# Kernel tuning notes

Measured on AMD Instinct MI355X. Metric: run time of the kernel, lower is better.

Reference implementation:

```python
import jax, jax.numpy as jnp
import numpy as np

DIM = 512  # word_hidden_size * 2


def _linear_params(key, din, dout, scale=0.05):
    kw, kb = jax.random.split(key)
    W = jax.random.normal(kw, (din, dout), dtype=jnp.float32) * scale
    b = jax.random.normal(kb, (dout,), dtype=jnp.float32) * scale
    return W, b


def setup_inputs() -> dict:
    key = jax.random.key(0)
    ks = jax.random.split(key, 16)
    S_c, S_q, B = 256, 32, 32
    inp = {
        'context_output': jax.random.normal(ks[0], (S_c, B, DIM), dtype=jnp.float32),
        'question_output': jax.random.normal(ks[1], (S_q, B, DIM), dtype=jnp.float32),
        'question_hidden_state': jax.random.normal(ks[2], (B, DIM), dtype=jnp.float32),
        'image_output': jax.random.normal(ks[3], (S_c, B, DIM), dtype=jnp.float32),
    }
    names = ['fc1', 'fc2', 'dm', 'rm', 'qm', 'rr', 'rg', 'qg']
    for i, n in enumerate(names):
        W, b = _linear_params(ks[4 + i], DIM, DIM)
        inp['W_' + n] = W
        inp['b_' + n] = b
    W_ms, b_ms = _linear_params(ks[12], DIM, 1)
    inp['W_ms'] = W_ms
    inp['b_ms'] = b_ms
    return inp


def reference(context_output, question_output, question_hidden_state, image_output,
              W_fc1, b_fc1, W_fc2, b_fc2, W_dm, b_dm, W_rm, b_rm, W_qm, b_qm,
              W_rr, b_rr, W_rg, b_rg, W_qg, b_qg, W_ms, b_ms):
    # ctx: [B, S, D] = fc1(context) + fc2(image) after seq-first -> batch-first permute
    ctx = (jnp.einsum('sbd,de->bse', context_output, W_fc1) + b_fc1
           + jnp.einsum('sbd,de->bse', image_output, W_fc2) + b_fc2)
    # hoist loop-invariant linear_dm(ctx): same math, computed once
    ctx_dm = jnp.einsum('bsd,de->bse', ctx, W_dm) + b_dm  # [B, S, D]

    B = ctx.shape[0]
    r0 = jnp.zeros((B, DIM), dtype=ctx.dtype)

    def step(r, q_t):  # r: [B, D], q_t: [B, D]
        rm = r @ W_rm + b_rm          # [B, D]
        qm = q_t @ W_qm + b_qm        # [B, D]
        m = jnp.tanh(ctx_dm + rm[:, None, :] + qm[:, None, :])  # [B, S, D]
        logits = jnp.einsum('bsd,do->bso', m, W_ms)[..., 0] + b_ms[0]  # [B, S]
        s = jax.nn.softmax(logits, axis=1)                     # [B, S]
        r_new = jnp.einsum('bs,bsd->bd', s, ctx) + jnp.tanh(r @ W_rr + b_rr)
        return r_new, None

    r, _ = jax.lax.scan(step, r0, question_output)  # scan over question tokens

    g = (r @ W_rg + b_rg) + (question_hidden_state @ W_qg + b_qg)  # [B, D]
    return g
```

## Files before the change

### kernel.cpp

```cpp
#include <hip/hip_runtime.h>
#include <hip/hip_bf16.h>

#define DIMD 512
#define NB   32
#define NS   256
#define NT   32
#define SA_STR  66
#define SCT_STR 258
#define SR_STR  132

typedef __bf16 bf16x8 __attribute__((ext_vector_type(8)));
typedef float  f32x4  __attribute__((ext_vector_type(4)));
typedef unsigned long long u64;

__device__ __forceinline__ float tanh_fast(float x) {
    float e = __expf(2.f * x);
    return 1.f - 2.f / (e + 1.f);
}

__device__ __forceinline__ void gl_lds16(const __bf16* g, __bf16* l) {
    __builtin_amdgcn_global_load_lds((const __attribute__((address_space(1))) void*)g,
                                     (__attribute__((address_space(3))) void*)l, 16, 0, 0);
}

__device__ __forceinline__ void pub64(u64* p, float v, unsigned tag) {
    u64 pk = ((u64)__float_as_uint(v) << 32) | (u64)tag;
    __hip_atomic_store(p, pk, __ATOMIC_RELAXED, __HIP_MEMORY_SCOPE_AGENT);
}
__device__ __forceinline__ float poll64(const u64* p, unsigned tag) {
    u64 v = __hip_atomic_load(p, __ATOMIC_RELAXED, __HIP_MEMORY_SCOPE_AGENT);
    while ((unsigned)v != tag) {
        __builtin_amdgcn_s_sleep(1);
        v = __hip_atomic_load(p, __ATOMIC_RELAXED, __HIP_MEMORY_SCOPE_AGENT);
    }
    return __uint_as_float((unsigned)(v >> 32));
}

__global__ void k_prep_all(const float* __restrict__ ctxin, const float* __restrict__ img,
                           const float* __restrict__ qin,
                           const float* __restrict__ Wfc1, const float* __restrict__ Wfc2,
                           const float* __restrict__ Wdm, const float* __restrict__ Wqm,
                           const float* __restrict__ Wrm, const float* __restrict__ Wrr,
                           const float* __restrict__ Wrg, const float* __restrict__ Wqg,
                           __bf16* __restrict__ acat, __bf16* __restrict__ qp,
                           __bf16* __restrict__ wcatT, __bf16* __restrict__ wdmT,
                           __bf16* __restrict__ wqmT, __bf16* __restrict__ wrmT,
                           __bf16* __restrict__ wrrT, __bf16* __restrict__ wrgT,
                           __bf16* __restrict__ wqgT) {
    int row = blockIdx.x;
    if (row < 8192) {
        int b = row >> 8, s = row & 255;
        const float* c  = ctxin + ((size_t)s * NB + b) * DIMD;
        const float* im = img   + ((size_t)s * NB + b) * DIMD;
        __bf16* o = acat + (size_t)row * 1024;
        for (int d = threadIdx.x; d < DIMD; d += 256) {
            o[d]       = (__bf16)c[d];
            o[512 + d] = (__bf16)im[d];
        }
    } else if (row < 10240) {
        int idx = (row - 8192) * 256 + threadIdx.x;
        qp[idx] = (__bf16)qin[idx];
    } else {
        __shared__ float tile[32][33];
        int zz = (row - 10240) >> 8;
        int idx = (row - 10240) & 255;
        int bx = idx & 15, by = idx >> 4;
        int x = threadIdx.x & 31, y = threadIdx.x >> 5;
        const float* src = (zz == 0) ? Wfc1 : (zz == 1) ? Wfc2 : (zz == 2) ? Wdm
                         : (zz == 3) ? Wqm : (zz == 4) ? Wrm : (zz == 5) ? Wrr
                         : (zz == 6) ? Wrg : Wqg;
        __bf16* dst; int stride, off;
        if (zz < 2) { dst = wcatT; stride = 1024; off = zz * 512; }
        else {
            dst = (zz == 2) ? wdmT : (zz == 3) ? wqmT : (zz == 4) ? wrmT
                : (zz == 5) ? wrrT : (zz == 6) ? wrgT : wqgT;
            stride = 512; off = 0;
        }
        int c0 = bx * 32, r0 = by * 32;
#pragma unroll
        for (int k = 0; k < 32; k += 8)
            tile[y + k][x] = src[(size_t)(r0 + y + k) * DIMD + c0 + x];
        __syncthreads();
#pragma unroll
        for (int k = 0; k < 32; k += 8)
            dst[(size_t)(c0 + y + k) * stride + off + r0 + x] = (__bf16)tile[x][y + k];
    }
}

__device__ __forceinline__ void gemm_tile128(const __bf16* __restrict__ A,
                                             const __bf16* __restrict__ BT,
                                             const float* __restrict__ bias1,
                                             const float* __restrict__ bias2,
                                             void* __restrict__ out, int N, int K,
                                             int m0, int n0, int out_f32,
                                             __bf16* As, __bf16* Bs) {
    int tid = threadIdx.x, wave = tid >> 6, lane = tid & 63;
    int wm_ = wave >> 1, wn = wave & 1;
    int lr = lane & 15, lq = lane >> 4;

    f32x4 acc[4][4];
#pragma unroll
    for (int i = 0; i < 4; i++)
#pragma unroll
        for (int j = 0; j < 4; j++) acc[i][j] = (f32x4){0.f, 0.f, 0.f, 0.f};

    int g0 = (wave * 2 + 0) * 64 + lane;
    int g1 = (wave * 2 + 1) * 64 + lane;
    int r0_ = g0 >> 2, c0_ = g0 & 3;
    int r1_ = g1 >> 2, c1_ = g1 & 3;
    __bf16* la0 = As + (wave * 2 + 0) * 512;
    __bf16* la1 = As + (wave * 2 + 1) * 512;
    __bf16* lb0 = Bs + (wave * 2 + 0) * 512;
    __bf16* lb1 = Bs + (wave * 2 + 1) * 512;

    for (int kk = 0; kk < K; kk += 32) {
        gl_lds16(A  + (size_t)(m0 + r0_) * K + kk + c0_ * 8, la0);
        gl_lds16(A  + (size_t)(m0 + r1_) * K + kk + c1_ * 8, la1);
        gl_lds16(BT + (size_t)(n0 + r0_) * K + kk + c0_ * 8, lb0);
        gl_lds16(BT + (size_t)(n0 + r1_) * K + kk + c1_ * 8, lb1);
        __syncthreads();
        bf16x8 af[4], bfv[4];
#pragma unroll
        for (int i = 0; i < 4; i++)
            af[i] = *(const bf16x8*)(As + (wm_ * 64 + i * 16 + lr) * 32 + lq * 8);
#pragma unroll
        for (int j = 0; j < 4; j++)
            bfv[j] = *(const bf16x8*)(Bs + (wn * 64 + j * 16 + lr) * 32 + lq * 8);
#pragma unroll
        for (int i = 0; i < 4; i++)
#pragma unroll
            for (int j = 0; j < 4; j++)
                acc[i][j] = __builtin_amdgcn_mfma_f32_16x16x32_bf16(af[i], bfv[j], acc[i][j], 0, 0, 0);
        __syncthreads();
    }

#pragma unroll
    for (int i = 0; i < 4; i++)
#pragma unroll
        for (int j = 0; j < 4; j++) {
            int col = n0 + wn * 64 + j * 16 + lr;
            float bs = (bias1 ? bias1[col] : 0.f) + (bias2 ? bias2[col] : 0.f);
#pragma unroll
            for (int r = 0; r < 4; r++) {
                int row = m0 + wm_ * 64 + i * 16 + lq * 4 + r;
                float v = acc[i][j][r] + bs;
                if (out_f32) ((float*)out)[(size_t)row * N + col] = v;
                else         ((__bf16*)out)[(size_t)row * N + col] = (__bf16)v;
            }
        }
}

__global__ void k_gemm128(const __bf16* __restrict__ A, const __bf16* __restrict__ BT,
                          const float* __restrict__ bias1, const float* __restrict__ bias2,
                          void* __restrict__ out, int M, int N, int K, int out_f32) {
    __shared__ __bf16 As[128 * 32];
    __shared__ __bf16 Bs[128 * 32];
    gemm_tile128(A, BT, bias1, bias2, out, N, K, blockIdx.x * 128, blockIdx.y * 128, out_f32, As, Bs);
}

__global__ void k_fused(const __bf16* __restrict__ ctxb, const __bf16* __restrict__ wdmT,
                        const float* __restrict__ bdm, __bf16* __restrict__ ctxdm,
                        const __bf16* __restrict__ qp, const __bf16* __restrict__ wqmT,
                        const float* __restrict__ bqm, float* __restrict__ qmf,
                        __bf16* __restrict__ ctxT) {
    __shared__ __bf16 As[128 * 32];
    __shared__ __bf16 Bs[128 * 32];
    int bid = blockIdx.x;
    if (bid < 256) {
        gemm_tile128(ctxb, wdmT, bdm, nullptr, ctxdm, 512, 512,
                     (bid & 63) * 128, (bid >> 6) * 128, 0, As, Bs);
    } else if (bid < 288) {
        int b2 = bid - 256;
        gemm_tile128(qp, wqmT, bqm, nullptr, qmf, 512, 512,
                     (b2 & 7) * 128, (b2 >> 3) * 128, 1, As, Bs);
    } else {
        int b3 = bid - 288;
        int z = b3 >> 7, rest = b3 & 127;
        int c0 = (rest & 15) * 32, s0 = (rest >> 4) * 32;
        __bf16* tile = As;
        int x = threadIdx.x & 31, y = threadIdx.x >> 5;
        const __bf16* S = ctxb + (size_t)z * NS * DIMD;
        __bf16* D = ctxT + (size_t)z * DIMD * NS;
#pragma unroll
        for (int k = 0; k < 32; k += 8)
            tile[(y + k) * 33 + x] = S[(size_t)(s0 + y + k) * DIMD + c0 + x];
        __syncthreads();
#pragma unroll
        for (int k = 0; k < 32; k += 8)
            D[(size_t)(c0 + y + k) * NS + s0 + x] = tile[x * 33 + y + k];
    }
}

__global__ __launch_bounds__(512, 2) void k_scan(
    const __bf16* __restrict__ ctxdm,
    const __bf16* __restrict__ ctxT,
    const __bf16* __restrict__ wrmT,
    const __bf16* __restrict__ wrrT,
    const float* __restrict__ qmf,
    const float* __restrict__ wms, const float* __restrict__ brm,
    const float* __restrict__ brr,
    const float* __restrict__ qh,
    const __bf16* __restrict__ wrgT,
    const __bf16* __restrict__ wqgT,
    const float* __restrict__ brg, const float* __restrict__ bqg,
    u64* parts,
    u64* rpub,
    float* __restrict__ out) {
    int bid = blockIdx.x;
    int b = bid & 31, j = bid >> 5;
    int tid = threadIdx.x, wave = tid >> 6, lane = tid & 63;
    int g = lane >> 3, i = lane & 7;

    __shared__ __bf16 sA[256 * SA_STR];
    __shared__ __bf16 sCT[64 * SCT_STR];
    __shared__ float  sQ[NT * 64];
    __shared__ float  sq[512];
    __shared__ float  sp[256];
    __shared__ float  s4[4];
    __shared__ float  sps[8 * 68];
    __shared__ float  srm[64], sh[64];
    __shared__ float  sr4[4 * SR_STR];
    __shared__ float  sqh4[4 * SR_STR];
    __shared__ float  smv[512];

    for (int c = tid; c < 2048; c += 512) {
        int row = c >> 3, c8 = c & 7;
        *(bf16x8*)(sA + row * SA_STR + c8 * 8) =
            *(const bf16x8*)(ctxdm + ((size_t)(b * NS + row)) * DIMD + j * 64 + c8 * 8);
    }
    for (int c = tid; c < 2048; c += 512) {
        int col = c >> 5, s8 = c & 31;
        *(bf16x8*)(sCT + col * SCT_STR + s8 * 8) =
            *(const bf16x8*)(ctxT + ((size_t)(b * DIMD) + j * 64 + col) * NS + s8 * 8);
    }
    for (int c = tid; c < NT * 64; c += 512) {
        int tt = c >> 6, e = c & 63;
        sQ[c] = qmf[((size_t)tt * NB + b) * DIMD + j * 64 + e];
    }
    sqh4[(tid >> 7) * SR_STR + (tid & 127)] = qh[(size_t)b * DIMD + tid];
    int m = tid >> 8, cl = (tid >> 2) & 63, q = tid & 3;
    const __bf16* wp = (m ? wrrT : wrmT) + ((size_t)(j * 64 + cl)) * DIMD + q * 128;
    bf16x8 wreg[16];
#pragma unroll
    for (int u = 0; u < 16; u++) wreg[u] = *(const bf16x8*)(wp + u * 8);

    float wm[8];
#pragma unroll
    for (int u = 0; u < 8; u++) wm[u] = wms[j * 64 + i * 8 + u];
    if (tid < 64) {
        srm[tid] = brm[j * 64 + tid];
        sh[tid]  = tanh_fast(brr[j * 64 + tid]);
    }
    __syncthreads();

    for (int t = 0; t < NT; t++) {
        unsigned tag = (unsigned)(t + 1);
        float rq[8];
#pragma unroll
        for (int u = 0; u < 8; u++) rq[u] = srm[i * 8 + u] + sQ[t * 64 + i * 8 + u];
#pragma unroll
        for (int k = 0; k < 4; k++) {
            int s = wave * 32 + k * 8 + g;
            bf16x8 cv = *(const bf16x8*)(sA + s * SA_STR + i * 8);
            float a = 0.f;
#pragma unroll
            for (int u = 0; u < 8; u++)
                a += tanh_fast((float)cv[u] + rq[u]) * wm[u];
            a += __shfl_xor(a, 1); a += __shfl_xor(a, 2); a += __shfl_xor(a, 4);
            if (i == 0) pub64(&parts[(b * 8 + j) * NS + s], a, tag);
        }

        {
            int s = tid >> 1, jh = (tid & 1) * 4;
            const u64* p0 = &parts[(b * 8 + jh + 0) * NS + s];
            const u64* p1 = &parts[(b * 8 + jh + 1) * NS + s];
            const u64* p2 = &parts[(b * 8 + jh + 2) * NS + s];
            const u64* p3 = &parts[(b * 8 + jh + 3) * NS + s];
            u64 v0, v1, v2, v3;
            for (;;) {
                v0 = __hip_atomic_load(p0, __ATOMIC_RELAXED, __HIP_MEMORY_SCOPE_AGENT);
                v1 = __hip_atomic_load(p1, __ATOMIC_RELAXED, __HIP_MEMORY_SCOPE_AGENT);
                v2 = __hip_atomic_load(p2, __ATOMIC_RELAXED, __HIP_MEMORY_SCOPE_AGENT);
                v3 = __hip_atomic_load(p3, __ATOMIC_RELAXED, __HIP_MEMORY_SCOPE_AGENT);
                if ((unsigned)v0 == tag && (unsigned)v1 == tag &&
                    (unsigned)v2 == tag && (unsigned)v3 == tag) break;
                __builtin_amdgcn_s_sleep(1);
            }
            sq[tid] = __uint_as_float((unsigned)(v0 >> 32)) + __uint_as_float((unsigned)(v1 >> 32))
                    + __uint_as_float((unsigned)(v2 >> 32)) + __uint_as_float((unsigned)(v3 >> 32));
        }
        __syncthreads();
        float ev = 0.f;
        if (tid < NS) { ev = __expf(sq[2 * tid] + sq[2 * tid + 1]); sp[tid] = ev; }
#pragma unroll
        for (int off = 32; off; off >>= 1) ev += __shfl_xor(ev, off);
        if (tid < NS && lane == 0) s4[wave] = ev;
        __syncthreads();
        float inv = 1.f / (s4[0] + s4[1] + s4[2] + s4[3]);
        {
            const __bf16* cp = sCT + lane * SCT_STR + wave * 32;
            const float* pp = sp + wave * 32;
            float a = 0.f;
#pragma unroll
            for (int k = 0; k < 32; k += 8) {
                bf16x8 v = *(const bf16x8*)(cp + k);
#pragma unroll
                for (int u = 0; u < 8; u++) a = fmaf(pp[k + u], (float)v[u], a);
            }
            sps[wave * 68 + lane] = a;
        }
        __syncthreads();
        if (tid < 64) {
            float a = 0.f;
#pragma unroll
            for (int w2 = 0; w2 < 8; w2++) a += sps[w2 * 68 + tid];
            float rv = a * inv + sh[tid];
            pub64(&rpub[b * DIMD + j * 64 + tid], rv, tag);
        }

        sr4[(tid >> 7) * SR_STR + (tid & 127)] = poll64(&rpub[b * DIMD + tid], tag);
        __syncthreads();
        if (t < NT - 1) {
            const float* sv = sr4 + q * SR_STR;
            float a0 = 0.f, a1 = 0.f;
#pragma unroll
            for (int u = 0; u < 16; u += 2) {
                bf16x8 w0 = wreg[u], w1 = wreg[u + 1];
#pragma unroll
                for (int e = 0; e < 8; e++) {
                    a0 = fmaf(sv[u * 8 + e],     (float)w0[e], a0);
                    a1 = fmaf(sv[u * 8 + 8 + e], (float)w1[e], a1);
                }
            }
            smv[tid] = a0 + a1;
            __syncthreads();
            if (tid < 128) {
                int m2 = tid >> 6, cl3 = tid & 63;
                float a = smv[m2 * 256 + cl3 * 4] + smv[m2 * 256 + cl3 * 4 + 1]
                        + smv[m2 * 256 + cl3 * 4 + 2] + smv[m2 * 256 + cl3 * 4 + 3];
                int col = j * 64 + cl3;
                if (m2 == 0) srm[cl3] = a + brm[col];
                else         sh[cl3]  = tanh_fast(a + brr[col]);
            }
            __syncthreads();
        } else {
            const __bf16* wp2 = (m ? wqgT : wrgT) + ((size_t)(j * 64 + cl)) * DIMD + q * 128;
            const float* sv = (m ? sqh4 : sr4) + q * SR_STR;
            float a0 = 0.f, a1 = 0.f;
#pragma unroll
            for (int u = 0; u < 16; u += 2) {
                bf16x8 w0 = *(const bf16x8*)(wp2 + u * 8);
                bf16x8 w1 = *(const bf16x8*)(wp2 + u * 8 + 8);
#pragma unroll
                for (int e = 0; e < 8; e++) {
                    a0 = fmaf(sv[u * 8 + e],     (float)w0[e], a0);
                    a1 = fmaf(sv[u * 8 + 8 + e], (float)w1[e], a1);
                }
            }
            smv[tid] = a0 + a1;
            __syncthreads();
            if (tid < 64) {
                int col = j * 64 + tid;
                float a = brg[col] + bqg[col];
#pragma unroll
                for (int m2 = 0; m2 < 2; m2++)
#pragma unroll
                    for (int q2 = 0; q2 < 4; q2++)
                        a += smv[m2 * 256 + tid * 4 + q2];
                out[(size_t)b * DIMD + col] = a;
            }
        }
    }
}


extern "C" void kernel_launch(void* const* d_in, const int* in_sizes, int n_in,
                              void* d_out, int out_size, void* d_ws, size_t ws_size,
                              hipStream_t stream) {
    const float* ctx_in = (const float*)d_in[0];
    const float* q_in   = (const float*)d_in[1];
    const float* qh     = (const float*)d_in[2];
    const float* img    = (const float*)d_in[3];
    const float* W_fc1  = (const float*)d_in[4];
    const float* b_fc1  = (const float*)d_in[5];
    const float* W_fc2  = (const float*)d_in[6];
    const float* b_fc2  = (const float*)d_in[7];
    const float* W_dm   = (const float*)d_in[8];
    const float* b_dm   = (const float*)d_in[9];
    const float* W_rm   = (const float*)d_in[10];
    const float* b_rm   = (const float*)d_in[11];
    const float* W_qm   = (const float*)d_in[12];
    const float* b_qm   = (const float*)d_in[13];
    const float* W_rr   = (const float*)d_in[14];
    const float* b_rr   = (const float*)d_in[15];
    const float* W_rg   = (const float*)d_in[16];
    const float* b_rg   = (const float*)d_in[17];
    const float* W_qg   = (const float*)d_in[18];
    const float* b_qg   = (const float*)d_in[19];
    const float* W_ms   = (const float*)d_in[20];

    char* w = (char*)d_ws;
    __bf16* acat  = (__bf16*)w;  w += (size_t)8192 * 1024 * 2;
    __bf16* qp    = (__bf16*)w;  w += (size_t)1024 * 512 * 2;
    __bf16* wcatT = (__bf16*)w;  w += (size_t)512 * 1024 * 2;
    __bf16* wdmT  = (__bf16*)w;  w += (size_t)512 * 512 * 2;
    __bf16* wqmT  = (__bf16*)w;  w += (size_t)512 * 512 * 2;
    __bf16* wrmT  = (__bf16*)w;  w += (size_t)512 * 512 * 2;
    __bf16* wrrT  = (__bf16*)w;  w += (size_t)512 * 512 * 2;
    __bf16* wrgT  = (__bf16*)w;  w += (size_t)512 * 512 * 2;
    __bf16* wqgT  = (__bf16*)w;  w += (size_t)512 * 512 * 2;
    __bf16* ctxb  = (__bf16*)w;  w += (size_t)8192 * 512 * 2;
    __bf16* ctxdm = (__bf16*)w;  w += (size_t)8192 * 512 * 2;
    char* x = (char*)acat;
    __bf16* ctxT  = (__bf16*)x;  x += (size_t)NB * DIMD * NS * 2;
    float*  qmf   = (float*)x;   x += (size_t)1024 * 512 * 4;
    u64*    rpub  = (u64*)x;     x += (size_t)NB * DIMD * 8;
    u64*    parts = (u64*)x;     x += (size_t)NB * 8 * NS * 8;

    k_prep_all<<<12288, 256, 0, stream>>>(ctx_in, img, q_in, W_fc1, W_fc2, W_dm,
                                          W_qm, W_rm, W_rr, W_rg, W_qg, acat, qp,
                                          wcatT, wdmT, wqmT, wrmT, wrrT, wrgT, wqgT);
    k_gemm128<<<dim3(64, 4), 256, 0, stream>>>(acat, wcatT, b_fc1, b_fc2, ctxb, 8192, 512, 1024, 0);
    k_fused<<<4384, 256, 0, stream>>>(ctxb, wdmT, b_dm, ctxdm, qp, wqmT, b_qm, qmf, ctxT);
    k_scan<<<256, 512, 0, stream>>>(ctxdm, ctxT, wrmT, wrrT, qmf, W_ms,
                                    b_rm, b_rr, qh, wrgT, wqgT, b_rg, b_qg,
                                    parts, rpub, (float*)d_out);
}
```

Measured before the change: 433.6 us.

## Repartition scan blocks by sequence rows and reduce recurrent matvec via atomics

Each block in the scan kernel now owns 32 context rows across all 512 features instead of 64 features across all 256 rows. Per-row logits therefore come out of one wave and need a single publish and poll, rather than partial sums gathered from eight blocks. The r@W_rm and r@W_rr products are split by input slice: each block atomically adds its partial into global accumulators, then a per-batch token barrier signals completion. This aims to shorten the cross-block synchronisation chain on each step, at the cost of global float atomics, an extra memset, a new token handshake, and nondeterministic summation order.

```diff
diff --git a/kernel.cpp b/kernel.cpp
--- a/kernel.cpp
+++ b/kernel.cpp
@@ -5,7 +5,6 @@
 #define NB   32
 #define NS   256
 #define NT   32
-#define SA_STR  66
 #define SCT_STR 258
 #define SR_STR  132
 
@@ -205,93 +204,73 @@
     const float* __restrict__ brg, const float* __restrict__ bqg,
     u64* parts,
     u64* rpub,
+    u64* tok,
+    float* rmsum,
+    float* rrsum,
     float* __restrict__ out) {
     int bid = blockIdx.x;
     int b = bid & 31, j = bid >> 5;
     int tid = threadIdx.x, wave = tid >> 6, lane = tid & 63;
-    int g = lane >> 3, i = lane & 7;
-
-    __shared__ __bf16 sA[256 * SA_STR];
+
+    __shared__ __bf16 sA[32 * 512];
     __shared__ __bf16 sCT[64 * SCT_STR];
-    __shared__ float  sQ[NT * 64];
-    __shared__ float  sq[512];
-    __shared__ float  sp[256];
+    __shared__ float  srm[DIMD];
+    __shared__ float  sQt[DIMD];
+    __shared__ float  sp[NS];
     __shared__ float  s4[4];
     __shared__ float  sps[8 * 68];
-    __shared__ float  srm[64], sh[64];
+    __shared__ float  sh[64], srl[64];
     __shared__ float  sr4[4 * SR_STR];
     __shared__ float  sqh4[4 * SR_STR];
     __shared__ float  smv[512];
 
     for (int c = tid; c < 2048; c += 512) {
-        int row = c >> 3, c8 = c & 7;
-        *(bf16x8*)(sA + row * SA_STR + c8 * 8) =
-            *(const bf16x8*)(ctxdm + ((size_t)(b * NS + row)) * DIMD + j * 64 + c8 * 8);
+        int row = c >> 6, c8 = c & 63;
+        *(bf16x8*)(sA + row * 512 + c8 * 8) =
+            *(const bf16x8*)(ctxdm + ((size_t)(b * NS + j * 32 + row)) * DIMD + c8 * 8);
     }
     for (int c = tid; c < 2048; c += 512) {
         int col = c >> 5, s8 = c & 31;
         *(bf16x8*)(sCT + col * SCT_STR + s8 * 8) =
             *(const bf16x8*)(ctxT + ((size_t)(b * DIMD) + j * 64 + col) * NS + s8 * 8);
     }
-    for (int c = tid; c < NT * 64; c += 512) {
-        int tt = c >> 6, e = c & 63;
-        sQ[c] = qmf[((size_t)tt * NB + b) * DIMD + j * 64 + e];
-    }
     sqh4[(tid >> 7) * SR_STR + (tid & 127)] = qh[(size_t)b * DIMD + tid];
-    int m = tid >> 8, cl = (tid >> 2) & 63, q = tid & 3;
-    const __bf16* wp = (m ? wrrT : wrmT) + ((size_t)(j * 64 + cl)) * DIMD + q * 128;
-    bf16x8 wreg[16];
-#pragma unroll
-    for (int u = 0; u < 16; u++) wreg[u] = *(const bf16x8*)(wp + u * 8);
-
+    const __bf16* wpm = wrmT + (size_t)tid * DIMD + j * 64;
+    const __bf16* wpr = wrrT + (size_t)tid * DIMD + j * 64;
+    bf16x8 wregm[8], wregr[8];
+#pragma unroll
+    for (int u = 0; u < 8; u++) { wregm[u] = *(const bf16x8*)(wpm + u * 8);
+                                  wregr[u] = *(const bf16x8*)(wpr + u * 8); }
     float wm[8];
 #pragma unroll
-    for (int u = 0; u < 8; u++) wm[u] = wms[j * 64 + i * 8 + u];
-    if (tid < 64) {
-        srm[tid] = brm[j * 64 + tid];
-        sh[tid]  = tanh_fast(brr[j * 64 + tid]);
-    }
+    for (int u = 0; u < 8; u++) wm[u] = wms[lane * 8 + u];
+
+    srm[tid] = brm[tid];
+    if (tid < 64) sh[tid] = tanh_fast(brr[j * 64 + tid]);
+    sQt[tid] = qmf[(size_t)b * DIMD + tid];
     __syncthreads();
 
     for (int t = 0; t < NT; t++) {
         unsigned tag = (unsigned)(t + 1);
         float rq[8];
 #pragma unroll
-        for (int u = 0; u < 8; u++) rq[u] = srm[i * 8 + u] + sQ[t * 64 + i * 8 + u];
+        for (int u = 0; u < 8; u++) rq[u] = srm[lane * 8 + u] + sQt[lane * 8 + u];
 #pragma unroll
         for (int k = 0; k < 4; k++) {
-            int s = wave * 32 + k * 8 + g;
-            bf16x8 cv = *(const bf16x8*)(sA + s * SA_STR + i * 8);
+            int row = wave * 4 + k;
+            bf16x8 cv = *(const bf16x8*)(sA + row * 512 + lane * 8);
             float a = 0.f;
 #pragma unroll
             for (int u = 0; u < 8; u++)
                 a += tanh_fast((float)cv[u] + rq[u]) * wm[u];
-            a += __shfl_xor(a, 1); a += __shfl_xor(a, 2); a += __shfl_xor(a, 4);
-            if (i == 0) pub64(&parts[(b * 8 + j) * NS + s], a, tag);
-        }
-
-        {
-            int s = tid >> 1, jh = (tid & 1) * 4;
-            const u64* p0 = &parts[(b * 8 + jh + 0) * NS + s];
-            const u64* p1 = &parts[(b * 8 + jh + 1) * NS + s];
-            const u64* p2 = &parts[(b * 8 + jh + 2) * NS + s];
-            const u64* p3 = &parts[(b * 8 + jh + 3) * NS + s];
-            u64 v0, v1, v2, v3;
-            for (;;) {
-                v0 = __hip_atomic_load(p0, __ATOMIC_RELAXED, __HIP_MEMORY_SCOPE_AGENT);
-                v1 = __hip_atomic_load(p1, __ATOMIC_RELAXED, __HIP_MEMORY_SCOPE_AGENT);
-                v2 = __hip_atomic_load(p2, __ATOMIC_RELAXED, __HIP_MEMORY_SCOPE_AGENT);
-                v3 = __hip_atomic_load(p3, __ATOMIC_RELAXED, __HIP_MEMORY_SCOPE_AGENT);
-                if ((unsigned)v0 == tag && (unsigned)v1 == tag &&
-                    (unsigned)v2 == tag && (unsigned)v3 == tag) break;
-                __builtin_amdgcn_s_sleep(1);
-            }
-            sq[tid] = __uint_as_float((unsigned)(v0 >> 32)) + __uint_as_float((unsigned)(v1 >> 32))
-                    + __uint_as_float((unsigned)(v2 >> 32)) + __uint_as_float((unsigned)(v3 >> 32));
-        }
-        __syncthreads();
+#pragma unroll
+            for (int off = 32; off; off >>= 1) a += __shfl_xor(a, off);
+            if (lane == 0) pub64(&parts[b * NS + j * 32 + row], a, tag);
+        }
+
         float ev = 0.f;
-        if (tid < NS) { ev = __expf(sq[2 * tid] + sq[2 * tid + 1]); sp[tid] = ev; }
+        if (tid < NS) { float lg = poll64(&parts[b * NS + tid], tag);
+                        ev = __expf(lg); sp[tid] = ev; }
 #pragma unroll
         for (int off = 32; off; off >>= 1) ev += __shfl_xor(ev, off);
         if (tid < NS && lane == 0) s4[wave] = ev;
@@ -315,35 +294,48 @@
 #pragma unroll
             for (int w2 = 0; w2 < 8; w2++) a += sps[w2 * 68 + tid];
             float rv = a * inv + sh[tid];
-            pub64(&rpub[b * DIMD + j * 64 + tid], rv, tag);
-        }
-
-        sr4[(tid >> 7) * SR_STR + (tid & 127)] = poll64(&rpub[b * DIMD + tid], tag);
-        __syncthreads();
+            srl[tid] = rv;
+            if (t == NT - 1) pub64(&rpub[b * DIMD + j * 64 + tid], rv, tag);
+        }
+        __syncthreads();
+
         if (t < NT - 1) {
-            const float* sv = sr4 + q * SR_STR;
-            float a0 = 0.f, a1 = 0.f;
-#pragma unroll
-            for (int u = 0; u < 16; u += 2) {
-                bf16x8 w0 = wreg[u], w1 = wreg[u + 1];
-#pragma unroll
-                for (int e = 0; e < 8; e++) {
-                    a0 = fmaf(sv[u * 8 + e],     (float)w0[e], a0);
-                    a1 = fmaf(sv[u * 8 + 8 + e], (float)w1[e], a1);
+            float am = 0.f, ar = 0.f;
+#pragma unroll
+            for (int u = 0; u < 8; u++) {
+                bf16x8 w0 = wregm[u], w1 = wregr[u];
+#pragma unroll
+                for (int e2 = 0; e2 < 8; e2++) {
+                    float rv = srl[u * 8 + e2];
+                    am = fmaf(rv, (float)w0[e2], am);
+                    ar = fmaf(rv, (float)w1[e2], ar);
                 }
             }
-            smv[tid] = a0 + a1;
+            __hip_atomic_fetch_add(&rmsum[((size_t)t * NB + b) * DIMD + tid], am,
+                                   __ATOMIC_RELAXED, __HIP_MEMORY_SCOPE_AGENT);
+            __hip_atomic_fetch_add(&rrsum[((size_t)t * NB + b) * DIMD + tid], ar,
+                                   __ATOMIC_RELAXED, __HIP_MEMORY_SCOPE_AGENT);
             __syncthreads();
-            if (tid < 128) {
-                int m2 = tid >> 6, cl3 = tid & 63;
-                float a = smv[m2 * 256 + cl3 * 4] + smv[m2 * 256 + cl3 * 4 + 1]
-                        + smv[m2 * 256 + cl3 * 4 + 2] + smv[m2 * 256 + cl3 * 4 + 3];
-                int col = j * 64 + cl3;
-                if (m2 == 0) srm[cl3] = a + brm[col];
-                else         sh[cl3]  = tanh_fast(a + brr[col]);
-            }
+            if (tid == 0) {
+                __atomic_signal_fence(__ATOMIC_SEQ_CST);
+                __builtin_amdgcn_s_waitcnt(0x0F70);
+                __atomic_signal_fence(__ATOMIC_SEQ_CST);
+                pub64(&tok[b * 8 + j], 0.f, tag);
+            }
+            if (tid < 8) poll64(&tok[b * 8 + tid], tag);
+            __syncthreads();
+            srm[tid] = brm[tid] + __hip_atomic_load(&rmsum[((size_t)t * NB + b) * DIMD + tid],
+                                                    __ATOMIC_RELAXED, __HIP_MEMORY_SCOPE_AGENT);
+            if (tid < 64)
+                sh[tid] = tanh_fast(brr[j * 64 + tid] +
+                          __hip_atomic_load(&rrsum[((size_t)t * NB + b) * DIMD + j * 64 + tid],
+                                            __ATOMIC_RELAXED, __HIP_MEMORY_SCOPE_AGENT));
+            sQt[tid] = qmf[((size_t)(t + 1) * NB + b) * DIMD + tid];
             __syncthreads();
         } else {
+            sr4[(tid >> 7) * SR_STR + (tid & 127)] = poll64(&rpub[b * DIMD + tid], tag);
+            __syncthreads();
+            int m = tid >> 8, cl = (tid >> 2) & 63, q = tid & 3;
             const __bf16* wp2 = (m ? wqgT : wrgT) + ((size_t)(j * 64 + cl)) * DIMD + q * 128;
             const float* sv = (m ? sqh4 : sr4) + q * SR_STR;
             float a0 = 0.f, a1 = 0.f;
@@ -352,9 +344,9 @@
                 bf16x8 w0 = *(const bf16x8*)(wp2 + u * 8);
                 bf16x8 w1 = *(const bf16x8*)(wp2 + u * 8 + 8);
 #pragma unroll
-                for (int e = 0; e < 8; e++) {
-                    a0 = fmaf(sv[u * 8 + e],     (float)w0[e], a0);
-                    a1 = fmaf(sv[u * 8 + 8 + e], (float)w1[e], a1);
+                for (int e2 = 0; e2 < 8; e2++) {
+                    a0 = fmaf(sv[u * 8 + e2],     (float)w0[e2], a0);
+                    a1 = fmaf(sv[u * 8 + 8 + e2], (float)w1[e2], a1);
                 }
             }
             smv[tid] = a0 + a1;
@@ -414,15 +406,19 @@
     char* x = (char*)acat;
     __bf16* ctxT  = (__bf16*)x;  x += (size_t)NB * DIMD * NS * 2;
     float*  qmf   = (float*)x;   x += (size_t)1024 * 512 * 4;
+    u64*    parts = (u64*)x;     x += (size_t)NB * NS * 8;
     u64*    rpub  = (u64*)x;     x += (size_t)NB * DIMD * 8;
-    u64*    parts = (u64*)x;     x += (size_t)NB * 8 * NS * 8;
+    u64*    tok   = (u64*)x;     x += (size_t)NB * 8 * 8;
+    float*  rmsum = (float*)x;   x += (size_t)(NT - 1) * NB * DIMD * 4;
+    float*  rrsum = (float*)x;   x += (size_t)(NT - 1) * NB * DIMD * 4;
 
     k_prep_all<<<12288, 256, 0, stream>>>(ctx_in, img, q_in, W_fc1, W_fc2, W_dm,
                                           W_qm, W_rm, W_rr, W_rg, W_qg, acat, qp,
                                           wcatT, wdmT, wqmT, wrmT, wrrT, wrgT, wqgT);
     k_gemm128<<<dim3(64, 4), 256, 0, stream>>>(acat, wcatT, b_fc1, b_fc2, ctxb, 8192, 512, 1024, 0);
     k_fused<<<4384, 256, 0, stream>>>(ctxb, wdmT, b_dm, ctxdm, qp, wqmT, b_qm, qmf, ctxT);
+    hipMemsetAsync(rmsum, 0, (size_t)2 * (NT - 1) * NB * DIMD * 4, stream);
     k_scan<<<256, 512, 0, stream>>>(ctxdm, ctxT, wrmT, wrrT, qmf, W_ms,
                                     b_rm, b_rr, qh, wrgT, wqgT, b_rg, b_qg,
-                                    parts, rpub, (float*)d_out);
-}
+                                    parts, rpub, tok, rmsum, rrsum, (float*)d_out);
+}
```

After: 432.6 us. Within noise of the previous version (-0.2%).
